# Kernel optimization log

Measured on AMD Instinct MI355X. Metric: run time of the kernel, lower is better.

Reference implementation:

```python
import jax, jax.numpy as jnp
import numpy as np

HIDDEN_DIM = 2048
NUM_EXPERTS = 8
TOP_K = 2
SCORE_SCALE_FACTOR = 1.0
TOKENS = 8192  # batch_size in the original 2D input


def setup_inputs() -> dict:
    key = jax.random.key(0)
    k1, k2, k3 = jax.random.split(key, 3)
    hidden_states = jax.random.normal(k1, (TOKENS, HIDDEN_DIM), dtype=jnp.float32)
    # nn.Linear weights (out_features, in_features), Kaiming-uniform-like scale
    gate_w = jax.random.normal(k2, (NUM_EXPERTS, HIDDEN_DIM), dtype=jnp.float32) / np.float32(np.sqrt(HIDDEN_DIM))
    expert_w = jax.random.normal(k3, (NUM_EXPERTS, HIDDEN_DIM, HIDDEN_DIM), dtype=jnp.float32) / np.float32(np.sqrt(HIDDEN_DIM))
    return {"hidden_states": hidden_states, "gate_w": gate_w, "expert_w": expert_w}


def reference(hidden_states, gate_w, expert_w):
    # router: logits = x @ W_gate^T, softmax in float32 (matches F.softmax(dtype=torch.float))
    router_logits = hidden_states @ gate_w.T                      # [T, E]
    routing_probs = jax.nn.softmax(router_logits.astype(jnp.float32), axis=-1)
    top_w, top_i = jax.lax.top_k(routing_probs, TOP_K)            # [T, K]
    top_w = top_w / jnp.sum(top_w, axis=-1, keepdims=True)        # renormalize over top-k
    top_w = top_w.astype(hidden_states.dtype)

    T = hidden_states.shape[0]
    # dense combine weights [T, E]: zero for unselected experts -> exactly the
    # gather-GEMM-scatter math (full capacity, no dropped tokens)
    combine = jnp.zeros((T, NUM_EXPERTS), dtype=hidden_states.dtype)
    combine = combine.at[jnp.arange(T)[:, None], top_i].set(top_w)

    # out[t,h] = scale * sum_e combine[t,e] * (x[t,:] @ expert_w[e]^T)[h]
    final_hidden_states = jnp.einsum('td,ehd,te->th', hidden_states, expert_w, combine) * SCORE_SCALE_FACTOR
    return final_hidden_states, router_logits
```

## Files before the change

kernel.cpp:

```cpp
#include <hip/hip_runtime.h>
#include <hip/hip_bf16.h>
#include <stdint.h>

#define TOKENS 8192
#define HD     2048
#define NE     8

typedef __attribute__((ext_vector_type(8)))  short short8;
typedef __attribute__((ext_vector_type(8)))  unsigned short ushort8v;
typedef __attribute__((ext_vector_type(4)))  float f32x4;
typedef __attribute__((ext_vector_type(16))) float f32x16;

__device__ __forceinline__ unsigned short f2bf_rne(float f) {
  union { float f; unsigned u; } v; v.f = f;
  unsigned u = v.u;
  return (unsigned short)((u + 0x7fffu + ((u >> 16) & 1u)) >> 16);
}

__device__ __forceinline__ void async_load16(const void* g, void* lds) {
  __builtin_amdgcn_global_load_lds(
      (const __attribute__((address_space(1))) unsigned int*)g,
      (__attribute__((address_space(3))) unsigned int*)lds, 16, 0, 0);
}

__global__ __launch_bounds__(256) void prep_kernel(
    const float* __restrict__ x, const float* __restrict__ gw,
    const float* __restrict__ ew, unsigned short* __restrict__ xb,
    unsigned short* __restrict__ wb, float* __restrict__ logits_out) {
  if (blockIdx.x >= 2048) {
    int i = (blockIdx.x - 2048) * 256 + threadIdx.x;
    const int n8 = NE * HD * HD / 8;
    const int stride = 4096 * 256;
    const float4* s4 = (const float4*)ew;
    ushort8v* d8 = (ushort8v*)wb;
    for (; i < n8; i += stride) {
      float4 a = s4[i * 2], b = s4[i * 2 + 1];
      ushort8v o;
      o[0] = f2bf_rne(a.x); o[1] = f2bf_rne(a.y);
      o[2] = f2bf_rne(a.z); o[3] = f2bf_rne(a.w);
      o[4] = f2bf_rne(b.x); o[5] = f2bf_rne(b.y);
      o[6] = f2bf_rne(b.z); o[7] = f2bf_rne(b.w);
      d8[i] = o;
    }
    return;
  }
  const int wid  = threadIdx.x >> 6;
  const int lane = threadIdx.x & 63;
  const int t = blockIdx.x * 4 + wid;

  const float4* xr = (const float4*)(x + (size_t)t * HD);
  const float4* g4 = (const float4*)gw;
  ushort4* xb4 = (ushort4*)(xb + (size_t)t * HD);

  float acc[NE];
#pragma unroll
  for (int e = 0; e < NE; ++e) acc[e] = 0.f;

#pragma unroll
  for (int it = 0; it < 8; ++it) {
    int idx = it * 64 + lane;
    float4 v = xr[idx];
    ushort4 o;
    o.x = f2bf_rne(v.x); o.y = f2bf_rne(v.y);
    o.z = f2bf_rne(v.z); o.w = f2bf_rne(v.w);
    xb4[idx] = o;
#pragma unroll
    for (int e = 0; e < NE; ++e) {
      float4 g = g4[e * 512 + idx];
      acc[e] += v.x * g.x + v.y * g.y + v.z * g.z + v.w * g.w;
    }
  }
#pragma unroll
  for (int e = 0; e < NE; ++e) {
#pragma unroll
    for (int off = 32; off > 0; off >>= 1)
      acc[e] += __shfl_xor(acc[e], off, 64);
  }
  if (lane == 0) {
    float* lo = logits_out + (size_t)t * NE;
#pragma unroll
    for (int e = 0; e < NE; ++e) lo[e] = acc[e];
  }
}

__global__ __launch_bounds__(1024) void bucket_kernel(
    const float* __restrict__ logits, int* __restrict__ counts,
    int* __restrict__ btok, float* __restrict__ bwt) {
  const int e = blockIdx.x;
  __shared__ int lcount;
  if (threadIdx.x == 0) lcount = 0;
  __syncthreads();
  const int lane = threadIdx.x & 63;

  for (int base = 0; base < TOKENS; base += 1024) {
    int t = base + threadIdx.x;
    const float* lo = logits + (size_t)t * NE;
    float l[NE];
#pragma unroll
    for (int k = 0; k < NE; ++k) l[k] = lo[k];
    int i0 = 0; float b0 = l[0];
#pragma unroll
    for (int k = 1; k < NE; ++k) if (l[k] > b0) { b0 = l[k]; i0 = k; }
    int i1 = -1; float b1 = -3.4e38f;
#pragma unroll
    for (int k = 0; k < NE; ++k) if (k != i0 && l[k] > b1) { b1 = l[k]; i1 = k; }
    float w0 = 1.f / (1.f + __expf(b1 - b0));
    float w1 = 1.f - w0;
#pragma unroll
    for (int s = 0; s < 2; ++s) {
      int  ex = s ? i1 : i0;
      float w = s ? w1 : w0;
      bool p = (ex == e);
      unsigned long long mask = __ballot(p);
      int prefix = __popcll(mask & ((1ull << lane) - 1ull));
      int tot    = __popcll(mask);
      int wb = 0;
      if (lane == 0 && tot) wb = atomicAdd(&lcount, tot);
      wb = __shfl(wb, 0, 64);
      if (p) {
        btok[e * TOKENS + wb + prefix] = t | (s << 13);
        bwt [e * TOKENS + wb + prefix] = w;
      }
    }
  }
  __syncthreads();
  if (threadIdx.x == 0) counts[e * 32] = lcount;
}

__global__ __launch_bounds__(256, 4) void moe_gemm_kernel(
    const unsigned short* __restrict__ xb,
    const unsigned short* __restrict__ wb,
    const int* __restrict__ counts,
    const int* __restrict__ btok,
    const float* __restrict__ bwt,
    float* __restrict__ out,
    unsigned short* __restrict__ slot1) {
  int d = blockIdx.x;
  int e, coltile, rowtile;
  if (d < 2048) {
    e       = d & 7;
    rowtile = (d >> 3) & 15;
    coltile = d >> 7;
  } else {
    int u = d - 2048;
    e       = u & 7;
    coltile = (u & 127) >> 3;
    rowtile = 16 + (u >> 7);
  }
  const int cnt = counts[e * 32];
  if (rowtile * 128 >= cnt) return;

  __shared__ unsigned short As[128 * 64];
  __shared__ unsigned short Bs[128 * 64];

  const int tid  = threadIdx.x;
  const int wid  = tid >> 6;
  const int lane = tid & 63;

  int a_off[4], b_off[4];
#pragma unroll
  for (int it = 0; it < 4; ++it) {
    int slot = wid * 256 + it * 64 + lane;
    int row  = slot >> 3;
    int ch   = (slot & 7) ^ (row & 7);
    int rc   = rowtile * 128 + row;
    rc = rc < cnt ? rc : cnt - 1;
    a_off[it] = (btok[e * TOKENS + rc] & (TOKENS - 1)) * HD + ch * 8;
    b_off[it] = (e * HD + coltile * 128 + row) * HD + ch * 8;
  }

  f32x16 acc[2][2];
#pragma unroll
  for (int i = 0; i < 2; ++i)
#pragma unroll
    for (int j = 0; j < 2; ++j)
#pragma unroll
      for (int r = 0; r < 16; ++r) acc[i][j][r] = 0.f;

  const int l5  = lane >> 5;
  const int ln  = lane & 31;
  const int wm2 = wid >> 1;
  const int wn2 = wid & 1;

  int a_rd[2][4], b_rd[2][4];
#pragma unroll
  for (int t = 0; t < 2; ++t)
#pragma unroll
    for (int kc = 0; kc < 4; ++kc) {
      int ra = wm2 * 64 + t * 32 + ln;
      a_rd[t][kc] = ra * 64 + ((kc * 2 + l5) ^ (ra & 7)) * 8;
      int rb = wn2 * 64 + t * 32 + ln;
      b_rd[t][kc] = rb * 64 + ((kc * 2 + l5) ^ (rb & 7)) * 8;
    }

  for (int k0 = 0; k0 < HD; k0 += 64) {
#pragma unroll
    for (int it = 0; it < 4; ++it) {
      async_load16(xb + a_off[it] + k0, &As[(wid * 256 + it * 64) * 8]);
      async_load16(wb + b_off[it] + k0, &Bs[(wid * 256 + it * 64) * 8]);
    }
    __syncthreads();
    short8 fa[2][4], fb[2][4];
#pragma unroll
    for (int t = 0; t < 2; ++t)
#pragma unroll
      for (int kc = 0; kc < 4; ++kc) {
        fa[t][kc] = *(const short8*)&As[a_rd[t][kc]];
        fb[t][kc] = *(const short8*)&Bs[b_rd[t][kc]];
      }
#pragma unroll
    for (int kc = 0; kc < 4; ++kc)
#pragma unroll
      for (int i = 0; i < 2; ++i)
#pragma unroll
        for (int j = 0; j < 2; ++j)
          acc[i][j] = __builtin_amdgcn_mfma_f32_32x32x16_bf16(
              fa[i][kc], fb[j][kc], acc[i][j], 0, 0, 0);
    __syncthreads();
  }

#pragma unroll
  for (int ti = 0; ti < 2; ++ti)
#pragma unroll
    for (int rg = 0; rg < 16; ++rg) {
      int row = (rg & 3) + 8 * (rg >> 2) + 4 * l5;
      int gm  = rowtile * 128 + wm2 * 64 + ti * 32 + row;
      if (gm < cnt) {
        int   dv = btok[e * TOKENS + gm];
        float w  = bwt [e * TOKENS + gm];
        int   nb = coltile * 128 + wn2 * 64 + ln;
        float v0 = w * acc[ti][0][rg];
        float v1 = w * acc[ti][1][rg];
        if (dv < TOKENS) {
          float* orow = out + (size_t)dv * HD + nb;
          orow[0]  = v0;
          orow[32] = v1;
        } else {
          unsigned short* srow = slot1 + (size_t)(dv - TOKENS) * HD + nb;
          srow[0]  = f2bf_rne(v0);
          srow[32] = f2bf_rne(v1);
        }
      }
    }
}

__global__ __launch_bounds__(256) void combine_kernel(
    const unsigned short* __restrict__ s1, float* __restrict__ out) {
  size_t u = (size_t)blockIdx.x * 256 + threadIdx.x;
  ushort8v sv = ((const ushort8v*)s1)[u];
  float4* o = (float4*)out + u * 2;
  float4 a = o[0], b = o[1];
  a.x += __uint_as_float((unsigned)sv[0] << 16);
  a.y += __uint_as_float((unsigned)sv[1] << 16);
  a.z += __uint_as_float((unsigned)sv[2] << 16);
  a.w += __uint_as_float((unsigned)sv[3] << 16);
  b.x += __uint_as_float((unsigned)sv[4] << 16);
  b.y += __uint_as_float((unsigned)sv[5] << 16);
  b.z += __uint_as_float((unsigned)sv[6] << 16);
  b.w += __uint_as_float((unsigned)sv[7] << 16);
  o[0] = a; o[1] = b;
}

extern "C" void kernel_launch(void* const* d_in, const int* in_sizes, int n_in,
                              void* d_out, int out_size, void* d_ws, size_t ws_size,
                              hipStream_t stream) {
  const float* x  = (const float*)d_in[0];
  const float* gw = (const float*)d_in[1];
  const float* ew = (const float*)d_in[2];
  float* out = (float*)d_out;

  char* ws = (char*)d_ws;
  unsigned short* xb    = (unsigned short*)ws;
  unsigned short* wb    = (unsigned short*)(ws + 33554432u);
  unsigned short* slot1 = (unsigned short*)(ws + 100663296u);
  int*   counts = (int*)(ws + 134217728u);
  int*   btok   = (int*)(ws + 134218752u);
  float* bwt    = (float*)(ws + 134480896u);

  float* logits = out + (size_t)TOKENS * HD;

  prep_kernel<<<6144, 256, 0, stream>>>(x, gw, ew, xb, wb, logits);
  bucket_kernel<<<NE, 1024, 0, stream>>>(logits, counts, btok, bwt);
  moe_gemm_kernel<<<4096, 256, 0, stream>>>(xb, wb, counts, btok, bwt, out, slot1);
  combine_kernel<<<8192, 256, 0, stream>>>(slot1, out);
}
```

Baseline: 465.9 us.

## Double-buffer MoE GEMM LDS tiles and parallelize routing bucket kernel

```diff
diff --git a/kernel.cpp b/kernel.cpp
--- a/kernel.cpp
+++ b/kernel.cpp
@@ -26,8 +26,10 @@
 __global__ __launch_bounds__(256) void prep_kernel(
     const float* __restrict__ x, const float* __restrict__ gw,
     const float* __restrict__ ew, unsigned short* __restrict__ xb,
-    unsigned short* __restrict__ wb, float* __restrict__ logits_out) {
+    unsigned short* __restrict__ wb, float* __restrict__ logits_out,
+    int* __restrict__ counts) {
   if (blockIdx.x >= 2048) {
+    if (blockIdx.x == 2048 && threadIdx.x < NE) counts[threadIdx.x * 32] = 0;
     int i = (blockIdx.x - 2048) * 256 + threadIdx.x;
     const int n8 = NE * HD * HD / 8;
     const int stride = 4096 * 256;
@@ -83,51 +85,43 @@
   }
 }
 
-__global__ __launch_bounds__(1024) void bucket_kernel(
+__global__ __launch_bounds__(256) void bucket_kernel(
     const float* __restrict__ logits, int* __restrict__ counts,
     int* __restrict__ btok, float* __restrict__ bwt) {
-  const int e = blockIdx.x;
-  __shared__ int lcount;
-  if (threadIdx.x == 0) lcount = 0;
-  __syncthreads();
+  const int e = blockIdx.x & 7;
+  const int t = (blockIdx.x >> 3) * 256 + threadIdx.x;
   const int lane = threadIdx.x & 63;
 
-  for (int base = 0; base < TOKENS; base += 1024) {
-    int t = base + threadIdx.x;
-    const float* lo = logits + (size_t)t * NE;
-    float l[NE];
-#pragma unroll
-    for (int k = 0; k < NE; ++k) l[k] = lo[k];
-    int i0 = 0; float b0 = l[0];
-#pragma unroll
-    for (int k = 1; k < NE; ++k) if (l[k] > b0) { b0 = l[k]; i0 = k; }
-    int i1 = -1; float b1 = -3.4e38f;
-#pragma unroll
-    for (int k = 0; k < NE; ++k) if (k != i0 && l[k] > b1) { b1 = l[k]; i1 = k; }
-    float w0 = 1.f / (1.f + __expf(b1 - b0));
-    float w1 = 1.f - w0;
-#pragma unroll
-    for (int s = 0; s < 2; ++s) {
-      int  ex = s ? i1 : i0;
-      float w = s ? w1 : w0;
-      bool p = (ex == e);
-      unsigned long long mask = __ballot(p);
-      int prefix = __popcll(mask & ((1ull << lane) - 1ull));
-      int tot    = __popcll(mask);
-      int wb = 0;
-      if (lane == 0 && tot) wb = atomicAdd(&lcount, tot);
-      wb = __shfl(wb, 0, 64);
-      if (p) {
-        btok[e * TOKENS + wb + prefix] = t | (s << 13);
-        bwt [e * TOKENS + wb + prefix] = w;
-      }
-    }
-  }
-  __syncthreads();
-  if (threadIdx.x == 0) counts[e * 32] = lcount;
-}
-
-__global__ __launch_bounds__(256, 4) void moe_gemm_kernel(
+  const float4* lo4 = (const float4*)(logits + (size_t)t * NE);
+  float4 la = lo4[0], lb = lo4[1];
+  float l[NE] = {la.x, la.y, la.z, la.w, lb.x, lb.y, lb.z, lb.w};
+  int i0 = 0; float b0 = l[0];
+#pragma unroll
+  for (int k = 1; k < NE; ++k) if (l[k] > b0) { b0 = l[k]; i0 = k; }
+  int i1 = -1; float b1 = -3.4e38f;
+#pragma unroll
+  for (int k = 0; k < NE; ++k) if (k != i0 && l[k] > b1) { b1 = l[k]; i1 = k; }
+  float w0 = 1.f / (1.f + __expf(b1 - b0));
+  float w1 = 1.f - w0;
+#pragma unroll
+  for (int s = 0; s < 2; ++s) {
+    int  ex = s ? i1 : i0;
+    float w = s ? w1 : w0;
+    bool p = (ex == e);
+    unsigned long long mask = __ballot(p);
+    int prefix = __popcll(mask & ((1ull << lane) - 1ull));
+    int tot    = __popcll(mask);
+    int wb = 0;
+    if (lane == 0 && tot) wb = atomicAdd(&counts[e * 32], tot);
+    wb = __shfl(wb, 0, 64);
+    if (p) {
+      btok[e * TOKENS + wb + prefix] = t | (s << 13);
+      bwt [e * TOKENS + wb + prefix] = w;
+    }
+  }
+}
+
+__global__ __launch_bounds__(256, 2) void moe_gemm_kernel(
     const unsigned short* __restrict__ xb,
     const unsigned short* __restrict__ wb,
     const int* __restrict__ counts,
@@ -150,14 +144,14 @@
   const int cnt = counts[e * 32];
   if (rowtile * 128 >= cnt) return;
 
-  __shared__ unsigned short As[128 * 64];
-  __shared__ unsigned short Bs[128 * 64];
+  __shared__ unsigned short As[2][128 * 64];
+  __shared__ unsigned short Bs[2][128 * 64];
 
   const int tid  = threadIdx.x;
   const int wid  = tid >> 6;
   const int lane = tid & 63;
 
-  int a_off[4], b_off[4];
+  int a_off[4], b_off[4], l_off[4];
 #pragma unroll
   for (int it = 0; it < 4; ++it) {
     int slot = wid * 256 + it * 64 + lane;
@@ -167,6 +161,7 @@
     rc = rc < cnt ? rc : cnt - 1;
     a_off[it] = (btok[e * TOKENS + rc] & (TOKENS - 1)) * HD + ch * 8;
     b_off[it] = (e * HD + coltile * 128 + row) * HD + ch * 8;
+    l_off[it] = (wid * 256 + it * 64) * 8;
   }
 
   f32x16 acc[2][2];
@@ -193,20 +188,37 @@
       b_rd[t][kc] = rb * 64 + ((kc * 2 + l5) ^ (rb & 7)) * 8;
     }
 
-  for (int k0 = 0; k0 < HD; k0 += 64) {
-#pragma unroll
-    for (int it = 0; it < 4; ++it) {
-      async_load16(xb + a_off[it] + k0, &As[(wid * 256 + it * 64) * 8]);
-      async_load16(wb + b_off[it] + k0, &Bs[(wid * 256 + it * 64) * 8]);
-    }
-    __syncthreads();
+#pragma unroll
+  for (int it = 0; it < 4; ++it) {
+    async_load16(xb + a_off[it], &As[0][l_off[it]]);
+    async_load16(wb + b_off[it], &Bs[0][l_off[it]]);
+  }
+
+  const int NT = HD / 64;
+  for (int kt = 0; kt < NT; ++kt) {
+    const int cur = kt & 1;
+    if (kt < NT - 1) {
+      const int nk0 = (kt + 1) * 64;
+#pragma unroll
+      for (int it = 0; it < 4; ++it) {
+        async_load16(xb + a_off[it] + nk0, &As[cur ^ 1][l_off[it]]);
+        async_load16(wb + b_off[it] + nk0, &Bs[cur ^ 1][l_off[it]]);
+      }
+      asm volatile("s_waitcnt vmcnt(8)" ::: "memory");
+    } else {
+      asm volatile("s_waitcnt vmcnt(0)" ::: "memory");
+    }
+    __builtin_amdgcn_sched_barrier(0);
+    __builtin_amdgcn_s_barrier();
+    __builtin_amdgcn_sched_barrier(0);
+
     short8 fa[2][4], fb[2][4];
 #pragma unroll
     for (int t = 0; t < 2; ++t)
 #pragma unroll
       for (int kc = 0; kc < 4; ++kc) {
-        fa[t][kc] = *(const short8*)&As[a_rd[t][kc]];
-        fb[t][kc] = *(const short8*)&Bs[b_rd[t][kc]];
+        fa[t][kc] = *(const short8*)&As[cur][a_rd[t][kc]];
+        fb[t][kc] = *(const short8*)&Bs[cur][b_rd[t][kc]];
       }
 #pragma unroll
     for (int kc = 0; kc < 4; ++kc)
@@ -216,7 +228,10 @@
         for (int j = 0; j < 2; ++j)
           acc[i][j] = __builtin_amdgcn_mfma_f32_32x32x16_bf16(
               fa[i][kc], fb[j][kc], acc[i][j], 0, 0, 0);
-    __syncthreads();
+
+    __builtin_amdgcn_sched_barrier(0);
+    __builtin_amdgcn_s_barrier();
+    __builtin_amdgcn_sched_barrier(0);
   }
 
 #pragma unroll
@@ -279,8 +294,8 @@
 
   float* logits = out + (size_t)TOKENS * HD;
 
-  prep_kernel<<<6144, 256, 0, stream>>>(x, gw, ew, xb, wb, logits);
-  bucket_kernel<<<NE, 1024, 0, stream>>>(logits, counts, btok, bwt);
+  prep_kernel<<<6144, 256, 0, stream>>>(x, gw, ew, xb, wb, logits, counts);
+  bucket_kernel<<<256, 256, 0, stream>>>(logits, counts, btok, bwt);
   moe_gemm_kernel<<<4096, 256, 0, stream>>>(xb, wb, counts, btok, bwt, out, slot1);
   combine_kernel<<<8192, 256, 0, stream>>>(slot1, out);
 }
```

Measured after the change: 508.7 us. 9.2% more time.
